# Performance work log

Hardware: AMD Instinct MI355X
Metric: run time of the kernel (lower is better)

Reference implementation:

```python
import jax, jax.numpy as jnp
import numpy as np
import math

KMAX = 4
K_FLOOR = 1e-6
NUM_GRAPHS = 32

def _k_lattice():
    r = np.arange(-KMAX, KMAX + 1)
    I, J, Kk = np.meshgrid(r, r, r, indexing='ij')
    lat = np.stack([I, J, Kk], axis=-1).reshape(-1, 3).astype(np.float32)
    lat = lat[np.any(lat != 0, axis=1)]  # exclude k=0 (include_k0=False)
    return jnp.asarray(lat)  # [K,3], K=728

def setup_inputs() -> dict:
    key = jax.random.key(0)
    ks = jax.random.split(key, 10)
    N, B, C, H = 8192, NUM_GRAPHS, 4, 64
    pos = jax.random.uniform(ks[0], (N, 3), dtype=jnp.float32) * 10.0
    batch = jnp.sort(jax.random.randint(ks[1], (N,), 0, B)).astype(jnp.int32)
    cell = jnp.eye(3, dtype=jnp.float32)[None] * 12.0 + 0.2 * jax.random.normal(ks[2], (B, 3, 3), dtype=jnp.float32)
    source = 0.1 * jax.random.normal(ks[3], (N, C), dtype=jnp.float32)
    W1 = jax.random.normal(ks[4], (3, H), dtype=jnp.float32) * (1.0 / math.sqrt(3))
    b1 = jnp.zeros((H,), jnp.float32)
    W2 = jax.random.normal(ks[5], (H, H), dtype=jnp.float32) * (1.0 / math.sqrt(H))
    b2 = jnp.zeros((H,), jnp.float32)
    W3 = jax.random.normal(ks[6], (H, 1), dtype=jnp.float32) * (1.0 / math.sqrt(H))
    b3 = jnp.zeros((1,), jnp.float32)
    return {"pos": pos, "batch": batch, "cell": cell, "source": source,
            "W1": W1, "b1": b1, "W2": W2, "b2": b2, "W3": W3, "b3": b3}

def reference(pos, batch, cell, source, W1, b1, W2, b2, W3, b3):
    two_pi = 2.0 * math.pi
    klat = _k_lattice()                              # [K,3]
    B = cell.shape[0]
    inv_cells = jnp.linalg.inv(cell)                 # [B,3,3]
    # fractional coords and phases
    frac = jnp.einsum('ni,nij->nj', pos, inv_cells[batch])   # [N,3]
    phases = two_pi * (frac @ klat.T)                # [N,K]
    cosP = jnp.cos(phases)
    sinP = jnp.sin(phases)
    # structure factors via segment-sum over graphs
    w_cos = source[:, None, :] * cosP[:, :, None]    # [N,K,C]
    w_sin = source[:, None, :] * sinP[:, :, None]
    S_cos = jax.ops.segment_sum(w_cos, batch, num_segments=B)  # [B,K,C]
    S_sin = jax.ops.segment_sum(w_sin, batch, num_segments=B)
    # k-space radial filter
    k_cart = two_pi * jnp.einsum('kd,bdh->bkh', klat, inv_cells)  # [B,K,3]
    k_norms = jnp.linalg.norm(k_cart, axis=-1)       # [B,K]
    safe_k = jnp.maximum(k_norms, K_FLOOR)
    x0 = jnp.log1p(safe_k)
    feat = jnp.stack([x0, x0 * x0, 1.0 / safe_k], axis=-1)       # [B,K,3]
    h = jax.nn.silu(feat @ W1 + b1)
    h = jax.nn.silu(h @ W2 + b2)
    scale = jax.nn.softplus((h @ W3 + b3)[..., 0])   # [B,K]
    w = (4.0 * math.pi / (safe_k * safe_k)) * scale
    w = jnp.where(k_norms > K_FLOOR, w, 0.0)         # include_k0=False
    volumes = jnp.maximum(jnp.abs(jnp.linalg.det(cell)), K_FLOOR)  # [B]
    # per-atom potential
    t_cos = w[batch] * cosP                          # [N,K]
    t_sin = w[batch] * sinP
    potential = (jnp.einsum('nk,nkc->nc', t_cos, S_cos[batch]) +
                 jnp.einsum('nk,nkc->nc', t_sin, S_sin[batch])) / volumes[batch][:, None]
    atom_energy = 0.5 * jnp.sum(source * potential, axis=-1, keepdims=True)  # [N,1]
    return atom_energy
```

## Files before the change

### kernel.cpp

```cpp
#include <hip/hip_runtime.h>
#include <math.h>

#define N_ATOMS 8192
#define NGRAPH  32
#define KHALF   364
#define TWO_PI  6.28318530717958647692f
#define CH 32

__device__ __forceinline__ float silu_f(float x) {
    return x / (1.0f + __expf(-x));
}

__device__ __forceinline__ int lower_bound_serial(const int* __restrict__ batch, int v) {
    int lo = 0, hi = N_ATOMS;
    while (lo < hi) {
        int mid = (lo + hi) >> 1;
        if (batch[mid] < v) lo = mid + 1; else hi = mid;
    }
    return lo;
}

__device__ __forceinline__ void inv3x3(const float* __restrict__ c, float* iv, float* detOut) {
    float a00 = c[0], a01 = c[1], a02 = c[2];
    float a10 = c[3], a11 = c[4], a12 = c[5];
    float a20 = c[6], a21 = c[7], a22 = c[8];
    float c00 = a11 * a22 - a12 * a21;
    float c01 = a12 * a20 - a10 * a22;
    float c02 = a10 * a21 - a11 * a20;
    float det = a00 * c00 + a01 * c01 + a02 * c02;
    float r = 1.0f / det;
    iv[0] = c00 * r; iv[1] = (a02 * a21 - a01 * a22) * r; iv[2] = (a01 * a12 - a02 * a11) * r;
    iv[3] = c01 * r; iv[4] = (a00 * a22 - a02 * a20) * r; iv[5] = (a02 * a10 - a00 * a12) * r;
    iv[6] = c02 * r; iv[7] = (a01 * a20 - a00 * a21) * r; iv[8] = (a00 * a11 - a01 * a10) * r;
    *detOut = det;
}

__device__ __forceinline__ int lower_bound_wave(const int* __restrict__ batch, int v, int lane) {
    int x = batch[lane * 128];
    int c1 = __popcll(__ballot(x < v));
    int lo2 = (c1 > 0 ? c1 - 1 : 0) * 128;
    int y = batch[lo2 + lane * 2];
    int c2 = __popcll(__ballot(y < v));
    if (c2 == 0) return lo2;
    int cand = lo2 + 2 * c2;
    return (batch[cand - 1] < v) ? cand : cand - 1;
}

__global__ __launch_bounds__(256) void kMain(
    const float* __restrict__ cell, const float* __restrict__ pos,
    const int* __restrict__ batch, const float* __restrict__ source,
    const float* __restrict__ W1, const float* __restrict__ b1,
    const float* __restrict__ W2, const float* __restrict__ b2,
    const float* __restrict__ W3, const float* __restrict__ b3,
    float* __restrict__ wbuf, float* __restrict__ ScQ, float* __restrict__ SsQ,
    float* __restrict__ atrigA, float* __restrict__ atrigB, int* __restrict__ startp)
{
    __shared__ float2 tab[CH][3][9];
    __shared__ float4 srcs[CH];
    __shared__ float4 partC[3][64];
    __shared__ float4 partS[3][64];
    __shared__ float  comb[256];
    __shared__ int    sbounds[2];

    int bid = blockIdx.x;
    int tid = threadIdx.x;

    if (bid < 91) {
        int w    = tid >> 6;
        int lane = tid & 63;
        int half = w & 1;
        int u = bid * 128 + (w >> 1) * 64 + lane;
        int b = u / KHALF;
        int k = u - b * KHALF;

        float iv[9]; float det;
        inv3x3(cell + b * 9, iv, &det);
        float vol = fmaxf(fabsf(det), 1e-6f);

        float fi = (float)(k / 81 - 4);
        float fj = (float)((k / 9) % 9 - 4);
        float fl = (float)(k % 9 - 4);
        float kx = TWO_PI * (fi * iv[0] + fj * iv[3] + fl * iv[6]);
        float ky = TWO_PI * (fi * iv[1] + fj * iv[4] + fl * iv[7]);
        float kz = TWO_PI * (fi * iv[2] + fj * iv[5] + fl * iv[8]);
        float kn = sqrtf(kx * kx + ky * ky + kz * kz);
        float sk = fmaxf(kn, 1e-6f);
        float x0 = log1pf(sk);
        float f0 = x0, f1 = x0 * x0, f2 = 1.0f / sk;

        float acc[32];
        #pragma unroll
        for (int j = 0; j < 32; ++j) acc[j] = b2[half * 32 + j];
        for (int i = 0; i < 64; ++i) {
            float a = b1[i] + f0 * W1[i] + f1 * W1[64 + i] + f2 * W1[128 + i];
            float h = silu_f(a);
            const float* w2row = W2 + i * 64 + half * 32;
            #pragma unroll
            for (int j = 0; j < 32; ++j) acc[j] = fmaf(h, w2row[j], acc[j]);
        }
        float partial = 0.f;
        #pragma unroll
        for (int j = 0; j < 32; ++j) partial += silu_f(acc[j]) * W3[half * 32 + j];

        comb[tid] = partial;
        __syncthreads();
        if (half == 0) {
            float mlp = b3[0] + partial + comb[tid + 64];
            float sc = (mlp > 20.0f) ? mlp : log1pf(__expf(mlp));
            float wgt = (12.566370614359172954f / (sk * sk)) * sc;
            if (!(kn > 1e-6f)) wgt = 0.0f;
            wbuf[u] = wgt / vol;
        }
        return;
    }

    if (bid == 859) {
        if (tid <= NGRAPH) startp[tid] = lower_bound_serial(batch, tid);
        return;
    }

    if (bid >= 860) {
        int n = (bid - 860) * 256 + tid;
        int bn = batch[n];
        float iv[9]; float det;
        inv3x3(cell + bn * 9, iv, &det);
        float px = pos[n * 3], py = pos[n * 3 + 1], pz = pos[n * 3 + 2];
        float p1 = TWO_PI * (px * iv[0] + py * iv[3] + pz * iv[6]);
        float p2 = TWO_PI * (px * iv[1] + py * iv[4] + pz * iv[7]);
        float p3 = TWO_PI * (px * iv[2] + py * iv[5] + pz * iv[8]);
        float s1, c1; sincosf(p1, &s1, &c1);
        float s2, c2; sincosf(p2, &s2, &c2);
        float s3, c3; sincosf(p3, &s3, &c3);
        float c3_2 = c3 * c3 - s3 * s3, s3_2 = 2.f * c3 * s3;
        float c3_4 = c3_2 * c3_2 - s3_2 * s3_2, s3_4 = 2.f * c3_2 * s3_2;
        ((float4*)atrigA)[n] = make_float4(c1, s1, c2, s2);
        ((float4*)atrigB)[n] = make_float4(c3, s3, c3_4, s3_4);
        return;
    }

    int sfid = bid - 91;
    int b = sfid / 24;
    int r = sfid - b * 24;
    int slice = r % 6;
    int q = r / 6;
    int kl = tid & 63;
    int h = tid >> 6;
    int k = slice * 64 + kl;
    bool kvalid = (k < KHALF);
    int kk = kvalid ? k : 0;
    int ip4 = kk / 81;
    int jp4 = (kk / 9) % 9;
    int lp4 = kk % 9;

    if (h < 2) {
        int lb = lower_bound_wave(batch, b + h, kl);
        if (kl == 0) sbounds[h] = lb;
    }
    __syncthreads();
    int s0 = sbounds[0], e0 = sbounds[1];

    int len = e0 - s0;
    int per = (len + 3) >> 2;
    int nb = s0 + q * per;
    int ne = min(nb + per, e0);

    float iv[9]; float det;
    inv3x3(cell + b * 9, iv, &det);

    float4 accC = make_float4(0.f, 0.f, 0.f, 0.f);
    float4 accS = make_float4(0.f, 0.f, 0.f, 0.f);

    for (int base = nb; base < ne; base += CH) {
        int cnt = min(CH, ne - base);
        __syncthreads();
        if (tid < 96) {
            int a = tid & 31, d = tid >> 5;
            if (a < cnt) {
                int n = base + a;
                float px = pos[n * 3], py = pos[n * 3 + 1], pz = pos[n * 3 + 2];
                float ph = TWO_PI * (px * iv[d] + py * iv[3 + d] + pz * iv[6 + d]);
                float s1, c1; sincosf(ph, &s1, &c1);
                float c2 = c1 * c1 - s1 * s1, s2 = 2.f * c1 * s1;
                float c3 = c2 * c1 - s2 * s1, s3 = c2 * s1 + s2 * c1;
                float c4 = c2 * c2 - s2 * s2, s4 = 2.f * c2 * s2;
                tab[a][d][4] = make_float2(1.f, 0.f);
                tab[a][d][5] = make_float2(c1, s1);
                tab[a][d][3] = make_float2(c1, -s1);
                tab[a][d][6] = make_float2(c2, s2);
                tab[a][d][2] = make_float2(c2, -s2);
                tab[a][d][7] = make_float2(c3, s3);
                tab[a][d][1] = make_float2(c3, -s3);
                tab[a][d][8] = make_float2(c4, s4);
                tab[a][d][0] = make_float2(c4, -s4);
            }
        } else if (tid < 128) {
            int a = tid - 96;
            if (a < cnt) srcs[a] = ((const float4*)source)[base + a];
        }
        __syncthreads();

        if (kvalid) {
            for (int a = h; a < cnt; a += 4) {
                float2 ti = tab[a][0][ip4];
                float2 tj = tab[a][1][jp4];
                float2 tl = tab[a][2][lp4];
                float c12 = ti.x * tj.x - ti.y * tj.y;
                float s12 = ti.x * tj.y + ti.y * tj.x;
                float cv = c12 * tl.x - s12 * tl.y;
                float sv = c12 * tl.y + s12 * tl.x;
                float4 s = srcs[a];
                accC.x = fmaf(s.x, cv, accC.x); accC.y = fmaf(s.y, cv, accC.y);
                accC.z = fmaf(s.z, cv, accC.z); accC.w = fmaf(s.w, cv, accC.w);
                accS.x = fmaf(s.x, sv, accS.x); accS.y = fmaf(s.y, sv, accS.y);
                accS.z = fmaf(s.z, sv, accS.z); accS.w = fmaf(s.w, sv, accS.w);
            }
        }
    }

    __syncthreads();
    if (h > 0) {
        partC[h - 1][kl] = accC;
        partS[h - 1][kl] = accS;
    }
    __syncthreads();
    if (h == 0 && kvalid) {
        #pragma unroll
        for (int qq = 0; qq < 3; ++qq) {
            float4 pc = partC[qq][kl], ps = partS[qq][kl];
            accC.x += pc.x; accC.y += pc.y; accC.z += pc.z; accC.w += pc.w;
            accS.x += ps.x; accS.y += ps.y; accS.z += ps.z; accS.w += ps.w;
        }
        ((float4*)ScQ)[q * (NGRAPH * KHALF) + b * KHALF + k] = accC;
        ((float4*)SsQ)[q * (NGRAPH * KHALF) + b * KHALF + k] = accS;
    }
}

__global__ __launch_bounds__(256) void kPot(
    const int* __restrict__ startp, const float* __restrict__ source,
    const float* __restrict__ wbuf,
    const float* __restrict__ ScQ, const float* __restrict__ SsQ,
    const float* __restrict__ atrigA, const float* __restrict__ atrigB,
    float* __restrict__ out)
{
    __shared__ float  lw[81];
    __shared__ float4 lSc[81];
    __shared__ float4 lSs[81];

    int b = blockIdx.x;
    int p = blockIdx.y;
    int zc = blockIdx.z;
    int ah = zc & 1;
    int at = zc >> 1;
    if (p == 4 && ah == 1) return;
    int tid = threadIdx.x;
    int j0 = ah ? 5 : 0;
    int j1 = ah ? 9 : 5;

    if (tid < 81) {
        int hk = p * 81 + tid;
        if (hk < KHALF) {
            int o = b * KHALF + hk;
            lw[tid] = wbuf[o];
            float4 c0 = ((const float4*)ScQ)[o];
            float4 c1 = ((const float4*)ScQ)[o + NGRAPH * KHALF];
            float4 c2 = ((const float4*)ScQ)[o + 2 * NGRAPH * KHALF];
            float4 c3 = ((const float4*)ScQ)[o + 3 * NGRAPH * KHALF];
            lSc[tid] = make_float4(c0.x + c1.x + c2.x + c3.x, c0.y + c1.y + c2.y + c3.y,
                                   c0.z + c1.z + c2.z + c3.z, c0.w + c1.w + c2.w + c3.w);
            float4 s0v = ((const float4*)SsQ)[o];
            float4 s1v = ((const float4*)SsQ)[o + NGRAPH * KHALF];
            float4 s2v = ((const float4*)SsQ)[o + 2 * NGRAPH * KHALF];
            float4 s3v = ((const float4*)SsQ)[o + 3 * NGRAPH * KHALF];
            lSs[tid] = make_float4(s0v.x + s1v.x + s2v.x + s3v.x, s0v.y + s1v.y + s2v.y + s3v.y,
                                   s0v.z + s1v.z + s2v.z + s3v.z, s0v.w + s1v.w + s2v.w + s3v.w);
        } else {
            lw[tid] = 0.f;
            lSc[tid] = make_float4(0.f, 0.f, 0.f, 0.f);
            lSs[tid] = make_float4(0.f, 0.f, 0.f, 0.f);
        }
    }
    __syncthreads();

    int s0 = startp[b];
    int e0 = startp[b + 1];
    int len = e0 - s0;
    int mid = s0 + ((len + 1) >> 1);
    int nb = at ? mid : s0;
    int ne = at ? e0 : mid;
    int g = 4 - p;

    for (int n = nb + tid; n < ne; n += 256) {
        float4 tA = ((const float4*)atrigA)[n];
        float4 tB = ((const float4*)atrigB)[n];
        float4 s  = ((const float4*)source)[n];
        float c1 = tA.x, s1 = tA.y, c2 = tA.z, s2 = tA.w;
        float c3 = tB.x, s3 = tB.y, c3_4 = tB.z, s3_4 = tB.w;

        float cg, sg;
        if (g == 0)      { cg = 1.f; sg = 0.f; }
        else if (g == 1) { cg = c1; sg = s1; }
        else {
            float c2p = c1 * c1 - s1 * s1, s2p = 2.f * c1 * s1;
            if (g == 2)      { cg = c2p; sg = s2p; }
            else if (g == 3) { cg = c2p * c1 - s2p * s1; sg = s2p * c1 + c2p * s1; }
            else             { cg = c2p * c2p - s2p * s2p; sg = 2.f * c2p * s2p; }
        }
        float ci0 = cg, si0 = -sg;

        float ejc, ejs;
        if (ah == 0) {
            float c2_2 = c2 * c2 - s2 * s2, s2_2 = 2.f * c2 * s2;
            float c2_4 = c2_2 * c2_2 - s2_2 * s2_2, s2_4 = 2.f * c2_2 * s2_2;
            ejc = ci0 * c2_4 + si0 * s2_4;
            ejs = si0 * c2_4 - ci0 * s2_4;
        } else {
            ejc = ci0 * c2 - si0 * s2;
            ejs = si0 * c2 + ci0 * s2;
        }

        float acc = 0.f;
        for (int jj = j0; jj < j1; ++jj) {
            float fc = ejc * c3_4 + ejs * s3_4;
            float fs = ejs * c3_4 - ejc * s3_4;
            #pragma unroll
            for (int ll = 0; ll < 9; ++ll) {
                int e = jj * 9 + ll;
                float4 C  = lSc[e];
                float4 S4 = lSs[e];
                float w = lw[e];
                float dc = s.x * C.x  + s.y * C.y  + s.z * C.z  + s.w * C.w;
                float ds = s.x * S4.x + s.y * S4.y + s.z * S4.z + s.w * S4.w;
                acc = fmaf(w, fmaf(fc, dc, fs * ds), acc);
                float nfc = fc * c3 - fs * s3;
                fs = fc * s3 + fs * c3;
                fc = nfc;
            }
            float nejc = ejc * c2 - ejs * s2;
            ejs = ejc * s2 + ejs * c2;
            ejc = nejc;
        }
        atomicAdd(&out[n], acc);
    }
}

extern "C" void kernel_launch(void* const* d_in, const int* in_sizes, int n_in,
                              void* d_out, int out_size, void* d_ws, size_t ws_size,
                              hipStream_t stream)
{
    const float* pos    = (const float*)d_in[0];
    const int*   batch  = (const int*)d_in[1];
    const float* cell   = (const float*)d_in[2];
    const float* source = (const float*)d_in[3];
    const float* W1 = (const float*)d_in[4];
    const float* b1 = (const float*)d_in[5];
    const float* W2 = (const float*)d_in[6];
    const float* b2 = (const float*)d_in[7];
    const float* W3 = (const float*)d_in[8];
    const float* b3 = (const float*)d_in[9];
    float* out = (float*)d_out;

    float* ws     = (float*)d_ws;
    float* wbuf   = ws;
    float* ScQ    = ws + 11648;
    float* SsQ    = ws + 198016;
    float* atrigA = ws + 384384;
    float* atrigB = ws + 417152;
    int*   startp = (int*)(ws + 449920);

    kMain<<<dim3(892), 256, 0, stream>>>(cell, pos, batch, source,
        W1, b1, W2, b2, W3, b3, wbuf, ScQ, SsQ, atrigA, atrigB, startp);
    kPot<<<dim3(NGRAPH, 5, 4), 256, 0, stream>>>(startp, source,
        wbuf, ScQ, SsQ, atrigA, atrigB, out);
}
```

Baseline: 106.2 us.

## Fuse k-filter MLP, structure factors and potential into one per-graph kernel

Merges the two kernels into one launch where each block owns a graph and a k-slice of up to 45 lattice points. The block computes its own MLP filter weights, structure factors over all atoms in the graph, and then the per-atom potential for half the atoms. This removes the workspace round trips, the second launch and the quarter-split partial sums. In exchange every block recomputes sincos for its atoms in both phases, scans the whole graph's atoms per slice, and uses an uneven 18-block-per-graph split.

```diff
diff --git a/kernel.cpp b/kernel.cpp
--- a/kernel.cpp
+++ b/kernel.cpp
@@ -5,19 +5,10 @@
 #define NGRAPH  32
 #define KHALF   364
 #define TWO_PI  6.28318530717958647692f
-#define CH 32
+
 
 __device__ __forceinline__ float silu_f(float x) {
     return x / (1.0f + __expf(-x));
-}
-
-__device__ __forceinline__ int lower_bound_serial(const int* __restrict__ batch, int v) {
-    int lo = 0, hi = N_ATOMS;
-    while (lo < hi) {
-        int mid = (lo + hi) >> 1;
-        if (batch[mid] < v) lo = mid + 1; else hi = mid;
-    }
-    return lo;
 }
 
 __device__ __forceinline__ void inv3x3(const float* __restrict__ c, float* iv, float* detOut) {
@@ -46,135 +37,107 @@
     return (batch[cand - 1] < v) ? cand : cand - 1;
 }
 
-__global__ __launch_bounds__(256) void kMain(
+__global__ __launch_bounds__(256) void kAll(
     const float* __restrict__ cell, const float* __restrict__ pos,
     const int* __restrict__ batch, const float* __restrict__ source,
     const float* __restrict__ W1, const float* __restrict__ b1,
     const float* __restrict__ W2, const float* __restrict__ b2,
     const float* __restrict__ W3, const float* __restrict__ b3,
-    float* __restrict__ wbuf, float* __restrict__ ScQ, float* __restrict__ SsQ,
-    float* __restrict__ atrigA, float* __restrict__ atrigB, int* __restrict__ startp)
+    float* __restrict__ out)
 {
-    __shared__ float2 tab[CH][3][9];
-    __shared__ float4 srcs[CH];
+    __shared__ float2 tab[64][3][9];
+    __shared__ float4 srcs[64];
     __shared__ float4 partC[3][64];
     __shared__ float4 partS[3][64];
     __shared__ float  comb[256];
     __shared__ int    sbounds[2];
+    __shared__ float  lw[45];
+    __shared__ float4 lSc[64];
+    __shared__ float4 lSs[64];
 
     int bid = blockIdx.x;
     int tid = threadIdx.x;
-
-    if (bid < 91) {
-        int w    = tid >> 6;
-        int lane = tid & 63;
-        int half = w & 1;
-        int u = bid * 128 + (w >> 1) * 64 + lane;
-        int b = u / KHALF;
-        int k = u - b * KHALF;
-
-        float iv[9]; float det;
-        inv3x3(cell + b * 9, iv, &det);
-        float vol = fmaxf(fabsf(det), 1e-6f);
-
-        float fi = (float)(k / 81 - 4);
-        float fj = (float)((k / 9) % 9 - 4);
-        float fl = (float)(k % 9 - 4);
-        float kx = TWO_PI * (fi * iv[0] + fj * iv[3] + fl * iv[6]);
-        float ky = TWO_PI * (fi * iv[1] + fj * iv[4] + fl * iv[7]);
-        float kz = TWO_PI * (fi * iv[2] + fj * iv[5] + fl * iv[8]);
-        float kn = sqrtf(kx * kx + ky * ky + kz * kz);
-        float sk = fmaxf(kn, 1e-6f);
-        float x0 = log1pf(sk);
-        float f0 = x0, f1 = x0 * x0, f2 = 1.0f / sk;
-
-        float acc[32];
-        #pragma unroll
-        for (int j = 0; j < 32; ++j) acc[j] = b2[half * 32 + j];
-        for (int i = 0; i < 64; ++i) {
-            float a = b1[i] + f0 * W1[i] + f1 * W1[64 + i] + f2 * W1[128 + i];
-            float h = silu_f(a);
-            const float* w2row = W2 + i * 64 + half * 32;
+    int gb  = bid / 18;
+    int rem = bid - gb * 18;
+    int p, ah, at;
+    if (rem < 16) { p = rem >> 2; ah = (rem >> 1) & 1; at = rem & 1; }
+    else          { p = 4; ah = 0; at = rem - 16; }
+    int j0   = ah ? 5 : 0;
+    int j1   = ah ? 9 : 5;
+    int nel  = ah ? 36 : 45;
+    int eoff = j0 * 9;
+
+    int kl = tid & 63;
+    int h  = tid >> 6;
+
+    if (h < 2) {
+        int lb = lower_bound_wave(batch, gb + h, kl);
+        if (kl == 0) sbounds[h] = lb;
+    }
+
+    float iv[9]; float det;
+    inv3x3(cell + gb * 9, iv, &det);
+    float vol = fmaxf(fabsf(det), 1e-6f);
+
+    {
+        float partial = 0.f, sk = 1.f, kn = 1.f;
+        bool evalid = false;
+        if (h < 2) {
+            int half = h;
+            int el = kl;
+            int hk = p * 81 + eoff + el;
+            evalid = (el < nel) && (hk < KHALF);
+            int ek = evalid ? hk : 0;
+            float fi = (float)(ek / 81 - 4);
+            float fj = (float)((ek / 9) % 9 - 4);
+            float fl = (float)(ek % 9 - 4);
+            float kx = TWO_PI * (fi * iv[0] + fj * iv[3] + fl * iv[6]);
+            float ky = TWO_PI * (fi * iv[1] + fj * iv[4] + fl * iv[7]);
+            float kz = TWO_PI * (fi * iv[2] + fj * iv[5] + fl * iv[8]);
+            kn = sqrtf(kx * kx + ky * ky + kz * kz);
+            sk = fmaxf(kn, 1e-6f);
+            float x0 = log1pf(sk);
+            float f0 = x0, f1 = x0 * x0, f2 = 1.0f / sk;
+
+            float acc[32];
             #pragma unroll
-            for (int j = 0; j < 32; ++j) acc[j] = fmaf(h, w2row[j], acc[j]);
-        }
-        float partial = 0.f;
-        #pragma unroll
-        for (int j = 0; j < 32; ++j) partial += silu_f(acc[j]) * W3[half * 32 + j];
-
-        comb[tid] = partial;
+            for (int j = 0; j < 32; ++j) acc[j] = b2[half * 32 + j];
+            for (int i = 0; i < 64; ++i) {
+                float a = b1[i] + f0 * W1[i] + f1 * W1[64 + i] + f2 * W1[128 + i];
+                float hh = silu_f(a);
+                const float* w2row = W2 + i * 64 + half * 32;
+                #pragma unroll
+                for (int j = 0; j < 32; ++j) acc[j] = fmaf(hh, w2row[j], acc[j]);
+            }
+            #pragma unroll
+            for (int j = 0; j < 32; ++j) partial += silu_f(acc[j]) * W3[half * 32 + j];
+            comb[tid] = partial;
+        }
         __syncthreads();
-        if (half == 0) {
+        if (h == 0) {
             float mlp = b3[0] + partial + comb[tid + 64];
             float sc = (mlp > 20.0f) ? mlp : log1pf(__expf(mlp));
             float wgt = (12.566370614359172954f / (sk * sk)) * sc;
             if (!(kn > 1e-6f)) wgt = 0.0f;
-            wbuf[u] = wgt / vol;
-        }
-        return;
-    }
-
-    if (bid == 859) {
-        if (tid <= NGRAPH) startp[tid] = lower_bound_serial(batch, tid);
-        return;
-    }
-
-    if (bid >= 860) {
-        int n = (bid - 860) * 256 + tid;
-        int bn = batch[n];
-        float iv[9]; float det;
-        inv3x3(cell + bn * 9, iv, &det);
-        float px = pos[n * 3], py = pos[n * 3 + 1], pz = pos[n * 3 + 2];
-        float p1 = TWO_PI * (px * iv[0] + py * iv[3] + pz * iv[6]);
-        float p2 = TWO_PI * (px * iv[1] + py * iv[4] + pz * iv[7]);
-        float p3 = TWO_PI * (px * iv[2] + py * iv[5] + pz * iv[8]);
-        float s1, c1; sincosf(p1, &s1, &c1);
-        float s2, c2; sincosf(p2, &s2, &c2);
-        float s3, c3; sincosf(p3, &s3, &c3);
-        float c3_2 = c3 * c3 - s3 * s3, s3_2 = 2.f * c3 * s3;
-        float c3_4 = c3_2 * c3_2 - s3_2 * s3_2, s3_4 = 2.f * c3_2 * s3_2;
-        ((float4*)atrigA)[n] = make_float4(c1, s1, c2, s2);
-        ((float4*)atrigB)[n] = make_float4(c3, s3, c3_4, s3_4);
-        return;
-    }
-
-    int sfid = bid - 91;
-    int b = sfid / 24;
-    int r = sfid - b * 24;
-    int slice = r % 6;
-    int q = r / 6;
-    int kl = tid & 63;
-    int h = tid >> 6;
-    int k = slice * 64 + kl;
-    bool kvalid = (k < KHALF);
-    int kk = kvalid ? k : 0;
-    int ip4 = kk / 81;
-    int jp4 = (kk / 9) % 9;
-    int lp4 = kk % 9;
-
-    if (h < 2) {
-        int lb = lower_bound_wave(batch, b + h, kl);
-        if (kl == 0) sbounds[h] = lb;
-    }
-    __syncthreads();
+            if (kl < nel) lw[kl] = evalid ? (wgt / vol) : 0.0f;
+        }
+    }
+
     int s0 = sbounds[0], e0 = sbounds[1];
 
-    int len = e0 - s0;
-    int per = (len + 3) >> 2;
-    int nb = s0 + q * per;
-    int ne = min(nb + per, e0);
-
-    float iv[9]; float det;
-    inv3x3(cell + b * 9, iv, &det);
+    bool kvalid = (kl < nel) && (p * 81 + eoff + kl < KHALF);
+    int eg  = eoff + (kvalid ? kl : 0);
+    int jp4 = eg / 9;
+    int lp4 = eg - jp4 * 9;
 
     float4 accC = make_float4(0.f, 0.f, 0.f, 0.f);
     float4 accS = make_float4(0.f, 0.f, 0.f, 0.f);
 
-    for (int base = nb; base < ne; base += CH) {
-        int cnt = min(CH, ne - base);
+    for (int base = s0; base < e0; base += 64) {
+        int cnt = min(64, e0 - base);
         __syncthreads();
-        if (tid < 96) {
-            int a = tid & 31, d = tid >> 5;
+        if (tid < 192) {
+            int a = tid & 63, d = tid >> 6;
             if (a < cnt) {
                 int n = base + a;
                 float px = pos[n * 3], py = pos[n * 3 + 1], pz = pos[n * 3 + 2];
@@ -193,15 +156,15 @@
                 tab[a][d][8] = make_float2(c4, s4);
                 tab[a][d][0] = make_float2(c4, -s4);
             }
-        } else if (tid < 128) {
-            int a = tid - 96;
+        } else {
+            int a = tid - 192;
             if (a < cnt) srcs[a] = ((const float4*)source)[base + a];
         }
         __syncthreads();
 
         if (kvalid) {
             for (int a = h; a < cnt; a += 4) {
-                float2 ti = tab[a][0][ip4];
+                float2 ti = tab[a][0][p];
                 float2 tj = tab[a][1][jp4];
                 float2 tl = tab[a][2][lp4];
                 float c12 = ti.x * tj.x - ti.y * tj.y;
@@ -223,66 +186,18 @@
         partS[h - 1][kl] = accS;
     }
     __syncthreads();
-    if (h == 0 && kvalid) {
+    if (h == 0) {
         #pragma unroll
         for (int qq = 0; qq < 3; ++qq) {
             float4 pc = partC[qq][kl], ps = partS[qq][kl];
             accC.x += pc.x; accC.y += pc.y; accC.z += pc.z; accC.w += pc.w;
             accS.x += ps.x; accS.y += ps.y; accS.z += ps.z; accS.w += ps.w;
         }
-        ((float4*)ScQ)[q * (NGRAPH * KHALF) + b * KHALF + k] = accC;
-        ((float4*)SsQ)[q * (NGRAPH * KHALF) + b * KHALF + k] = accS;
-    }
-}
-
-__global__ __launch_bounds__(256) void kPot(
-    const int* __restrict__ startp, const float* __restrict__ source,
-    const float* __restrict__ wbuf,
-    const float* __restrict__ ScQ, const float* __restrict__ SsQ,
-    const float* __restrict__ atrigA, const float* __restrict__ atrigB,
-    float* __restrict__ out)
-{
-    __shared__ float  lw[81];
-    __shared__ float4 lSc[81];
-    __shared__ float4 lSs[81];
-
-    int b = blockIdx.x;
-    int p = blockIdx.y;
-    int zc = blockIdx.z;
-    int ah = zc & 1;
-    int at = zc >> 1;
-    if (p == 4 && ah == 1) return;
-    int tid = threadIdx.x;
-    int j0 = ah ? 5 : 0;
-    int j1 = ah ? 9 : 5;
-
-    if (tid < 81) {
-        int hk = p * 81 + tid;
-        if (hk < KHALF) {
-            int o = b * KHALF + hk;
-            lw[tid] = wbuf[o];
-            float4 c0 = ((const float4*)ScQ)[o];
-            float4 c1 = ((const float4*)ScQ)[o + NGRAPH * KHALF];
-            float4 c2 = ((const float4*)ScQ)[o + 2 * NGRAPH * KHALF];
-            float4 c3 = ((const float4*)ScQ)[o + 3 * NGRAPH * KHALF];
-            lSc[tid] = make_float4(c0.x + c1.x + c2.x + c3.x, c0.y + c1.y + c2.y + c3.y,
-                                   c0.z + c1.z + c2.z + c3.z, c0.w + c1.w + c2.w + c3.w);
-            float4 s0v = ((const float4*)SsQ)[o];
-            float4 s1v = ((const float4*)SsQ)[o + NGRAPH * KHALF];
-            float4 s2v = ((const float4*)SsQ)[o + 2 * NGRAPH * KHALF];
-            float4 s3v = ((const float4*)SsQ)[o + 3 * NGRAPH * KHALF];
-            lSs[tid] = make_float4(s0v.x + s1v.x + s2v.x + s3v.x, s0v.y + s1v.y + s2v.y + s3v.y,
-                                   s0v.z + s1v.z + s2v.z + s3v.z, s0v.w + s1v.w + s2v.w + s3v.w);
-        } else {
-            lw[tid] = 0.f;
-            lSc[tid] = make_float4(0.f, 0.f, 0.f, 0.f);
-            lSs[tid] = make_float4(0.f, 0.f, 0.f, 0.f);
-        }
+        lSc[kl] = accC;
+        lSs[kl] = accS;
     }
     __syncthreads();
 
-    int s0 = startp[b];
-    int e0 = startp[b + 1];
     int len = e0 - s0;
     int mid = s0 + ((len + 1) >> 1);
     int nb = at ? mid : s0;
@@ -290,22 +205,27 @@
     int g = 4 - p;
 
     for (int n = nb + tid; n < ne; n += 256) {
-        float4 tA = ((const float4*)atrigA)[n];
-        float4 tB = ((const float4*)atrigB)[n];
-        float4 s  = ((const float4*)source)[n];
-        float c1 = tA.x, s1 = tA.y, c2 = tA.z, s2 = tA.w;
-        float c3 = tB.x, s3 = tB.y, c3_4 = tB.z, s3_4 = tB.w;
-
-        float cg, sg;
-        if (g == 0)      { cg = 1.f; sg = 0.f; }
-        else if (g == 1) { cg = c1; sg = s1; }
+        float px = pos[n * 3], py = pos[n * 3 + 1], pz = pos[n * 3 + 2];
+        float p1 = TWO_PI * (px * iv[0] + py * iv[3] + pz * iv[6]);
+        float p2 = TWO_PI * (px * iv[1] + py * iv[4] + pz * iv[7]);
+        float p3 = TWO_PI * (px * iv[2] + py * iv[5] + pz * iv[8]);
+        float s1, c1; sincosf(p1, &s1, &c1);
+        float s2, c2; sincosf(p2, &s2, &c2);
+        float s3, c3; sincosf(p3, &s3, &c3);
+        float c3_2 = c3 * c3 - s3 * s3, s3_2 = 2.f * c3 * s3;
+        float c3_4 = c3_2 * c3_2 - s3_2 * s3_2, s3_4 = 2.f * c3_2 * s3_2;
+        float4 s = ((const float4*)source)[n];
+
+        float cg_, sg_;
+        if (g == 0)      { cg_ = 1.f; sg_ = 0.f; }
+        else if (g == 1) { cg_ = c1; sg_ = s1; }
         else {
             float c2p = c1 * c1 - s1 * s1, s2p = 2.f * c1 * s1;
-            if (g == 2)      { cg = c2p; sg = s2p; }
-            else if (g == 3) { cg = c2p * c1 - s2p * s1; sg = s2p * c1 + c2p * s1; }
-            else             { cg = c2p * c2p - s2p * s2p; sg = 2.f * c2p * s2p; }
-        }
-        float ci0 = cg, si0 = -sg;
+            if (g == 2)      { cg_ = c2p; sg_ = s2p; }
+            else if (g == 3) { cg_ = c2p * c1 - s2p * s1; sg_ = s2p * c1 + c2p * s1; }
+            else             { cg_ = c2p * c2p - s2p * s2p; sg_ = 2.f * c2p * s2p; }
+        }
+        float ci0 = cg_, si0 = -sg_;
 
         float ejc, ejs;
         if (ah == 0) {
@@ -324,13 +244,13 @@
             float fs = ejs * c3_4 - ejc * s3_4;
             #pragma unroll
             for (int ll = 0; ll < 9; ++ll) {
-                int e = jj * 9 + ll;
-                float4 C  = lSc[e];
-                float4 S4 = lSs[e];
-                float w = lw[e];
+                int el = (jj - j0) * 9 + ll;
+                float4 C  = lSc[el];
+                float4 S4 = lSs[el];
+                float w_ = lw[el];
                 float dc = s.x * C.x  + s.y * C.y  + s.z * C.z  + s.w * C.w;
                 float ds = s.x * S4.x + s.y * S4.y + s.z * S4.z + s.w * S4.w;
-                acc = fmaf(w, fmaf(fc, dc, fs * ds), acc);
+                acc = fmaf(w_, fmaf(fc, dc, fs * ds), acc);
                 float nfc = fc * c3 - fs * s3;
                 fs = fc * s3 + fs * c3;
                 fc = nfc;
@@ -358,17 +278,8 @@
     const float* W3 = (const float*)d_in[8];
     const float* b3 = (const float*)d_in[9];
     float* out = (float*)d_out;
-
-    float* ws     = (float*)d_ws;
-    float* wbuf   = ws;
-    float* ScQ    = ws + 11648;
-    float* SsQ    = ws + 198016;
-    float* atrigA = ws + 384384;
-    float* atrigB = ws + 417152;
-    int*   startp = (int*)(ws + 449920);
-
-    kMain<<<dim3(892), 256, 0, stream>>>(cell, pos, batch, source,
-        W1, b1, W2, b2, W3, b3, wbuf, ScQ, SsQ, atrigA, atrigB, startp);
-    kPot<<<dim3(NGRAPH, 5, 4), 256, 0, stream>>>(startp, source,
-        wbuf, ScQ, SsQ, atrigA, atrigB, out);
-}
+    (void)d_ws; (void)ws_size;
+
+    kAll<<<dim3(NGRAPH * 18), 256, 0, stream>>>(cell, pos, batch, source,
+        W1, b1, W2, b2, W3, b3, out);
+}
```

Result: slower. 114.9 us (+8.2%).
